# Kernel tuning notes

Measured on AMD Instinct MI355X. Metric: run time of the kernel, lower is better.

## Reference

```python
import jax, jax.numpy as jnp
import numpy as np
from jax import lax


def setup_inputs() -> dict:
    key = jax.random.key(0)
    ks = jax.random.split(key, 8)
    B, N, q = 16, 4096, 256
    sc = float(1.0 / np.sqrt(q))
    return {
        "u": jax.random.normal(ks[0], (B, N, q), jnp.float32),
        "a": jax.random.normal(ks[1], (q,), jnp.float32),  # diag of A
        "W_B": jax.random.normal(ks[2], (q, q), jnp.float32) * sc,
        "b_B": jax.random.normal(ks[3], (q,), jnp.float32) * sc,
        "W_C": jax.random.normal(ks[4], (q, q), jnp.float32) * sc,
        "b_C": jax.random.normal(ks[5], (q,), jnp.float32) * sc,
        "W_D": jax.random.normal(ks[6], (q, q), jnp.float32) * sc,
        "b_D": jax.random.normal(ks[7], (q,), jnp.float32) * sc,
    }


def _solve_im(u, a, W_B, b_B, dt):
    """IM solver. A is diagonal, so M_inv is four diagonal blocks:
    new_x = s*x - dt*s*a*z ; new_z = dt*s*x + s*z, with s = 1/(1+dt^2*a).
    Forcing F = M_inv @ [dt*B(u); 0] -> (dt*s*Bu, dt^2*s*Bu)."""
    s = 1.0 / (1.0 + dt * dt * a)  # (q,)
    Bu = jnp.einsum("bnq,pq->bnp", u, W_B) + b_B  # (B,N,q), torch Linear: u @ W^T + b
    f_x = (dt * s) * Bu
    f_z = (dt * dt * s) * Bu
    dsa = dt * s * a
    ds = dt * s

    def step(carry, f):
        x, z = carry
        fx, fz = f
        x_new = s * x - dsa * z + fx
        z_new = ds * x + s * z + fz
        return (x_new, z_new), z_new

    Bsz, _, q = u.shape
    init = (jnp.zeros((Bsz, q), u.dtype), jnp.zeros((Bsz, q), u.dtype))
    # scan over time axis
    _, z_t = lax.scan(step, init, (jnp.moveaxis(f_x, 1, 0), jnp.moveaxis(f_z, 1, 0)))
    return jnp.moveaxis(z_t, 0, 1)  # (B,N,q) -- the out[..., size:] half


def reference(u, a, W_B, b_B, W_C, b_C, W_D, b_D):
    N = u.shape[1]
    dt = 1.0 / N
    y = _solve_im(u, a, W_B, b_B, dt)
    x = (jnp.einsum("bnq,pq->bnp", y, W_C) + b_C) + (jnp.einsum("bnq,pq->bnp", u, W_D) + b_D)
    x = jax.nn.gelu(x, approximate=False)  # torch GELU default = exact erf
    # GLU(concat([x, x], -1)) == x * sigmoid(x)
    out = x * jax.nn.sigmoid(x) + u
    return (out, y)
```

## Files before the change

kernel.cpp:

```cpp
#include <hip/hip_runtime.h>
#include <hip/hip_bf16.h>
#include <cstdint>

typedef __bf16 bf16_t;
typedef __bf16 bf16x8 __attribute__((ext_vector_type(8)));
typedef float f32x4 __attribute__((ext_vector_type(4)));

#define B_SZ 16
#define N_SZ 4096
#define Q_SZ 256
#define M_TOT (B_SZ * N_SZ)
#define DT (1.0f / 4096.0f)
#define LDST 40
#define CHUNKS 16
#define CLEN (N_SZ / CHUNKS)
#define PF 8


__device__ __forceinline__ bf16x8 load8f(const float* p) {
  const float4 v0 = *(const float4*)p;
  const float4 v1 = *(const float4*)(p + 4);
  bf16x8 v;
  v[0] = (bf16_t)v0.x; v[1] = (bf16_t)v0.y; v[2] = (bf16_t)v0.z; v[3] = (bf16_t)v0.w;
  v[4] = (bf16_t)v1.x; v[5] = (bf16_t)v1.y; v[6] = (bf16_t)v1.z; v[7] = (bf16_t)v1.w;
  return v;
}

__device__ __forceinline__ void gll16(const bf16_t* g, bf16_t* l) {
  __builtin_amdgcn_global_load_lds(
      (const __attribute__((address_space(1))) void*)g,
      (__attribute__((address_space(3))) void*)l, 16, 0, 0);
}


__device__ __forceinline__ void stage2(const bf16_t* __restrict__ A,
                                       const bf16_t* __restrict__ Bm,
                                       int m0, int n0, int k0, int t,
                                       bf16_t* As, bf16_t* Bs) {
#pragma unroll
  for (int j = 0; j < 2; ++j) {
    const int i = j * 256 + t;
    const int row = i >> 2;
    const int cpos = i & 3;
    const int cdat = cpos ^ ((row >> 1) & 3);
    bf16_t* la = As + (size_t)i * 8;
    bf16_t* lb = Bs + (size_t)i * 8;
    gll16(A + (size_t)(m0 + row) * Q_SZ + k0 + cdat * 8, la);
    gll16(Bm + (size_t)(n0 + row) * Q_SZ + k0 + cdat * 8, lb);
  }
}

__device__ __forceinline__ void mstep(const bf16_t* As, const bf16_t* Bs,
                                      int t, f32x4 acc[4][4]) {
  const int lane = t & 63, ln = lane & 15, quad = lane >> 4;
  const int wave = t >> 6;
  const int wm = (wave & 1) * 64, wn = (wave >> 1) * 64;
  const int csw = (quad ^ ((ln >> 1) & 3)) * 8;
  bf16x8 af[4], bv[4];
#pragma unroll
  for (int mi = 0; mi < 4; ++mi) {
    af[mi] = *(const bf16x8*)(As + (wm + mi * 16 + ln) * 32 + csw);
    bv[mi] = *(const bf16x8*)(Bs + (wn + mi * 16 + ln) * 32 + csw);
  }
#pragma unroll
  for (int mi = 0; mi < 4; ++mi)
#pragma unroll
    for (int ni = 0; ni < 4; ++ni)
      acc[mi][ni] = __builtin_amdgcn_mfma_f32_16x16x32_bf16(af[mi], bv[ni],
                                                            acc[mi][ni], 0, 0, 0);
}

__global__ __launch_bounds__(256) void prep_kernel(
    const float* __restrict__ u, const float* __restrict__ WB,
    const float* __restrict__ WC, const float* __restrict__ WD,
    bf16_t* __restrict__ ub, bf16_t* __restrict__ WBb,
    bf16_t* __restrict__ WCb, bf16_t* __restrict__ WDb) {
  const int g = blockIdx.x * 256 + threadIdx.x;
  const int UC = (M_TOT * Q_SZ) / 8;
  const float* src;
  bf16_t* dst;
  int idx;
  if (g < UC) {
    src = u; dst = ub; idx = g;
  } else {
    const int h = g - UC;
    const int w = h >> 13;
    idx = h & 8191;
    src = (w == 0) ? WB : (w == 1) ? WC : WD;
    dst = (w == 0) ? WBb : (w == 1) ? WCb : WDb;
  }
  *(bf16x8*)(dst + (size_t)idx * 8) = load8f(src + (size_t)idx * 8);
}

__global__ __launch_bounds__(256) void gemm1b_kernel(
    const bf16_t* __restrict__ ub, const bf16_t* __restrict__ WBb,
    const float* __restrict__ a, const float* __restrict__ bB,
    float* __restrict__ fx) {
  __shared__ __align__(16) bf16_t As[2][128 * 32];
  __shared__ __align__(16) bf16_t Bs[2][128 * 32];
  const int t = threadIdx.x;
  const int bid = blockIdx.x;
  const int swz = (bid & 7) * 128 + (bid >> 3);
  const int m0 = (swz >> 1) * 128, n0 = (swz & 1) * 128;
  f32x4 acc[4][4] = {};
  stage2(ub, WBb, m0, n0, 0, t, As[0], Bs[0]);
  __syncthreads();
#pragma unroll 2
  for (int k = 0; k < 8; ++k) {
    const int cur = k & 1;
    if (k < 7)
      stage2(ub, WBb, m0, n0, (k + 1) * 32, t, As[cur ^ 1], Bs[cur ^ 1]);
    mstep(As[cur], Bs[cur], t, acc);
    __syncthreads();
  }
  const int lane = t & 63, ln = lane & 15, quad = lane >> 4;
  const int wave = t >> 6;
  const int wm = (wave & 1) * 64, wn = (wave >> 1) * 64;
#pragma unroll
  for (int ni = 0; ni < 4; ++ni) {
    const int gp = n0 + wn + ni * 16 + ln;
    const float av = a[gp];
    const float s = 1.0f / (1.0f + DT * DT * av);
    const float sc = DT * s;
    const float bb = bB[gp];
#pragma unroll
    for (int mi = 0; mi < 4; ++mi) {
      const int gm = m0 + wm + mi * 16 + quad * 4;
#pragma unroll
      for (int r2 = 0; r2 < 4; ++r2)
        fx[(size_t)(gm + r2) * Q_SZ + gp] = sc * (acc[mi][ni][r2] + bb);
    }
  }
}

__global__ __launch_bounds__(256) void gemm2b_kernel(
    const bf16_t* __restrict__ yb, const bf16_t* __restrict__ WCb,
    const bf16_t* __restrict__ ub, const bf16_t* __restrict__ WDb,
    const float* __restrict__ u, const float* __restrict__ bC,
    const float* __restrict__ bD, float* __restrict__ out0) {
  __shared__ __align__(16) bf16_t As[2][128 * 32];
  __shared__ __align__(16) bf16_t Bs[2][128 * 32];
  const int t = threadIdx.x;
  const int bid = blockIdx.x;
  const int swz = (bid & 7) * 128 + (bid >> 3);
  const int m0 = (swz >> 1) * 128, n0 = (swz & 1) * 128;
  f32x4 acc[4][4] = {};
  stage2(yb, WCb, m0, n0, 0, t, As[0], Bs[0]);
  __syncthreads();
#pragma unroll 2
  for (int kk = 0; kk < 16; ++kk) {
    const int cur = kk & 1;
    if (kk < 15) {
      const int nk = kk + 1;
      const bf16_t* Ap = (nk < 8) ? yb : ub;
      const bf16_t* Bp = (nk < 8) ? WCb : WDb;
      stage2(Ap, Bp, m0, n0, (nk & 7) * 32, t, As[cur ^ 1], Bs[cur ^ 1]);
    }
    mstep(As[cur], Bs[cur], t, acc);
    __syncthreads();
  }
  const int lane = t & 63, ln = lane & 15, quad = lane >> 4;
  const int wave = t >> 6;
  const int wm = (wave & 1) * 64, wn = (wave >> 1) * 64;
#pragma unroll
  for (int ni = 0; ni < 4; ++ni) {
    const int gp = n0 + wn + ni * 16 + ln;
    const float bias = bC[gp] + bD[gp];
#pragma unroll
    for (int mi = 0; mi < 4; ++mi) {
      const int gm = m0 + wm + mi * 16 + quad * 4;
#pragma unroll
      for (int r2 = 0; r2 < 4; ++r2) {
        const float x = acc[mi][ni][r2] + bias;
        const float g = 0.5f * x * (1.0f + erff(x * 0.70710678118654752f));
        const float sg = 1.0f / (1.0f + __expf(-g));
        const float uu = u[(size_t)(gm + r2) * Q_SZ + gp];
        out0[(size_t)(gm + r2) * Q_SZ + gp] = fmaf(g, sg, uu);
      }
    }
  }
}


__global__ __launch_bounds__(256) void scan1_kernel(
    const float* __restrict__ fx, const float* __restrict__ a,
    float* __restrict__ ex, float* __restrict__ ez) {
  const int g = blockIdx.x * 256 + threadIdx.x;
  const int p = g & 255, c = (g >> 8) & (CHUNKS - 1), b = g >> 12;
  const float av = a[p];
  const float s = 1.0f / (1.0f + DT * DT * av);
  const float dsa = DT * s * av, dss = DT * s;
  float x = 0.f, z = 0.f;
  const float* fp = fx + ((size_t)b * N_SZ + c * CLEN) * Q_SZ + p;
  float buf[PF], nbuf[PF];
#pragma unroll
  for (int j = 0; j < PF; ++j) buf[j] = fp[(size_t)j * Q_SZ];
  for (int n = 0; n < CLEN; n += PF) {
    if (n + PF < CLEN) {
#pragma unroll
      for (int j = 0; j < PF; ++j) nbuf[j] = fp[(size_t)(n + PF + j) * Q_SZ];
    }
#pragma unroll
    for (int j = 0; j < PF; ++j) {
      const float f = buf[j];
      const float xn = fmaf(s, x, fmaf(-dsa, z, f));
      const float zn = fmaf(dss, x, fmaf(s, z, DT * f));
      x = xn; z = zn;
    }
#pragma unroll
    for (int j = 0; j < PF; ++j) buf[j] = nbuf[j];
  }
  ex[g] = x; ez[g] = z;
}

__global__ __launch_bounds__(256) void scan2_kernel(
    const float* __restrict__ a, const float* __restrict__ ex,
    const float* __restrict__ ez, float* __restrict__ ix, float* __restrict__ iz) {
  const int g = blockIdx.x * 256 + threadIdx.x;
  const int p = g & 255, b = g >> 8;
  const float av = a[p];
  const float s = 1.0f / (1.0f + DT * DT * av);
  float m00 = s, m01 = -DT * s * av, m10 = DT * s, m11 = s;
#pragma unroll
  for (int i = 0; i < 8; ++i) {
    const float a00 = fmaf(m00, m00, m01 * m10);
    const float a01 = m01 * (m00 + m11);
    const float a10 = m10 * (m00 + m11);
    const float a11 = fmaf(m11, m11, m01 * m10);
    m00 = a00; m01 = a01; m10 = a10; m11 = a11;
  }
  float x = 0.f, z = 0.f;
  for (int c = 0; c < CHUNKS; ++c) {
    const size_t idx = ((size_t)b * CHUNKS + c) * Q_SZ + p;
    ix[idx] = x; iz[idx] = z;
    const float xn = fmaf(m00, x, fmaf(m01, z, ex[idx]));
    const float zn = fmaf(m10, x, fmaf(m11, z, ez[idx]));
    x = xn; z = zn;
  }
}

__global__ __launch_bounds__(256) void scan3_kernel(
    const float* __restrict__ a, const float* __restrict__ ix,
    const float* __restrict__ iz, float* __restrict__ yf,
    bf16_t* __restrict__ yb) {
  const int g = blockIdx.x * 256 + threadIdx.x;
  const int p = g & 255, c = (g >> 8) & (CHUNKS - 1), b = g >> 12;
  const float av = a[p];
  const float s = 1.0f / (1.0f + DT * DT * av);
  const float dsa = DT * s * av, dss = DT * s;
  float x = ix[g], z = iz[g];
  const size_t base = ((size_t)b * N_SZ + c * CLEN) * Q_SZ + p;
  float* yp = yf + base;
  bf16_t* ybp = yb ? yb + base : nullptr;
  float buf[PF], nbuf[PF];
#pragma unroll
  for (int j = 0; j < PF; ++j) buf[j] = yp[(size_t)j * Q_SZ];
  for (int n = 0; n < CLEN; n += PF) {
    if (n + PF < CLEN) {
#pragma unroll
      for (int j = 0; j < PF; ++j) nbuf[j] = yp[(size_t)(n + PF + j) * Q_SZ];
    }
#pragma unroll
    for (int j = 0; j < PF; ++j) {
      const float f = buf[j];
      const float xn = fmaf(s, x, fmaf(-dsa, z, f));
      const float zn = fmaf(dss, x, fmaf(s, z, DT * f));
      x = xn; z = zn;
      yp[(size_t)(n + j) * Q_SZ] = zn;
      if (yb) ybp[(size_t)(n + j) * Q_SZ] = (bf16_t)zn;
    }
#pragma unroll
    for (int j = 0; j < PF; ++j) buf[j] = nbuf[j];
  }
}

__global__ __launch_bounds__(256) void scan_mono_kernel(
    const float* __restrict__ a, float* __restrict__ yf) {
  const int g = blockIdx.x * 256 + threadIdx.x;
  const int p = g & 255, b = g >> 8;
  const float av = a[p];
  const float s = 1.0f / (1.0f + DT * DT * av);
  const float dsa = DT * s * av, dss = DT * s;
  float x = 0.f, z = 0.f;
  float* yp = yf + (size_t)b * N_SZ * Q_SZ + p;
  float buf[PF], nbuf[PF];
#pragma unroll
  for (int j = 0; j < PF; ++j) buf[j] = yp[(size_t)j * Q_SZ];
  for (int n = 0; n < N_SZ; n += PF) {
    if (n + PF < N_SZ) {
#pragma unroll
      for (int j = 0; j < PF; ++j) nbuf[j] = yp[(size_t)(n + PF + j) * Q_SZ];
    }
#pragma unroll
    for (int j = 0; j < PF; ++j) {
      const float f = buf[j];
      const float xn = fmaf(s, x, fmaf(-dsa, z, f));
      const float zn = fmaf(dss, x, fmaf(s, z, DT * f));
      x = xn; z = zn;
      yp[(size_t)(n + j) * Q_SZ] = zn;
    }
#pragma unroll
    for (int j = 0; j < PF; ++j) buf[j] = nbuf[j];
  }
}


__device__ __forceinline__ void kloop(const float* __restrict__ Ap,
                                      const float* __restrict__ Bp,
                                      int m0, int n0, int t,
                                      bf16_t* As, bf16_t* Bs, f32x4 acc[4][4]) {
  const int r = t >> 2, cc = t & 3;
  const int lane = t & 63, ln = lane & 15, quad = lane >> 4;
  const int wave = t >> 6;
  const int wm = (wave & 1) * 64, wn = (wave >> 1) * 64;

  for (int k0 = 0; k0 < Q_SZ; k0 += 32) {
#pragma unroll
    for (int i = 0; i < 2; ++i) {
      const int row = r + i * 64;
      const int col = k0 + cc * 8;
      *(bf16x8*)(As + row * LDST + cc * 8) =
          load8f(Ap + (size_t)(m0 + row) * Q_SZ + col);
      *(bf16x8*)(Bs + row * LDST + cc * 8) =
          load8f(Bp + (size_t)(n0 + row) * Q_SZ + col);
    }
    __syncthreads();
    bf16x8 af[4], bv[4];
#pragma unroll
    for (int mi = 0; mi < 4; ++mi) {
      af[mi] = *(const bf16x8*)(As + (wm + mi * 16 + ln) * LDST + quad * 8);
      bv[mi] = *(const bf16x8*)(Bs + (wn + mi * 16 + ln) * LDST + quad * 8);
    }
#pragma unroll
    for (int mi = 0; mi < 4; ++mi)
#pragma unroll
      for (int ni = 0; ni < 4; ++ni)
        acc[mi][ni] = __builtin_amdgcn_mfma_f32_16x16x32_bf16(af[mi], bv[ni],
                                                              acc[mi][ni], 0, 0, 0);
    __syncthreads();
  }
}

__global__ __launch_bounds__(256) void gemm1_kernel(
    const float* __restrict__ u, const float* __restrict__ WB,
    const float* __restrict__ a, const float* __restrict__ bB,
    float* __restrict__ fx) {
  __shared__ __align__(16) bf16_t As[128 * LDST];
  __shared__ __align__(16) bf16_t Bs[128 * LDST];
  const int t = threadIdx.x;
  const int m0 = blockIdx.x * 128, n0 = blockIdx.y * 128;
  f32x4 acc[4][4] = {};
  kloop(u, WB, m0, n0, t, As, Bs, acc);

  const int lane = t & 63, ln = lane & 15, quad = lane >> 4;
  const int wave = t >> 6;
  const int wm = (wave & 1) * 64, wn = (wave >> 1) * 64;
#pragma unroll
  for (int ni = 0; ni < 4; ++ni) {
    const int gp = n0 + wn + ni * 16 + ln;
    const float av = a[gp];
    const float s = 1.0f / (1.0f + DT * DT * av);
    const float sc = DT * s;
    const float bb = bB[gp];
#pragma unroll
    for (int mi = 0; mi < 4; ++mi) {
      const int gm = m0 + wm + mi * 16 + quad * 4;
#pragma unroll
      for (int r2 = 0; r2 < 4; ++r2)
        fx[(size_t)(gm + r2) * Q_SZ + gp] = sc * (acc[mi][ni][r2] + bb);
    }
  }
}

__global__ __launch_bounds__(256) void gemm2_kernel(
    const float* __restrict__ y, const float* __restrict__ WC,
    const float* __restrict__ u, const float* __restrict__ WD,
    const float* __restrict__ bC, const float* __restrict__ bD,
    float* __restrict__ out0) {
  __shared__ __align__(16) bf16_t As[128 * LDST];
  __shared__ __align__(16) bf16_t Bs[128 * LDST];
  const int t = threadIdx.x;
  const int m0 = blockIdx.x * 128, n0 = blockIdx.y * 128;
  f32x4 acc[4][4] = {};
  kloop(y, WC, m0, n0, t, As, Bs, acc);
  kloop(u, WD, m0, n0, t, As, Bs, acc);

  const int lane = t & 63, ln = lane & 15, quad = lane >> 4;
  const int wave = t >> 6;
  const int wm = (wave & 1) * 64, wn = (wave >> 1) * 64;
#pragma unroll
  for (int ni = 0; ni < 4; ++ni) {
    const int gp = n0 + wn + ni * 16 + ln;
    const float bias = bC[gp] + bD[gp];
#pragma unroll
    for (int mi = 0; mi < 4; ++mi) {
      const int gm = m0 + wm + mi * 16 + quad * 4;
#pragma unroll
      for (int r2 = 0; r2 < 4; ++r2) {
        const float x = acc[mi][ni][r2] + bias;
        const float g = 0.5f * x * (1.0f + erff(x * 0.70710678118654752f));
        const float sg = 1.0f / (1.0f + __expf(-g));
        const float uu = u[(size_t)(gm + r2) * Q_SZ + gp];
        out0[(size_t)(gm + r2) * Q_SZ + gp] = fmaf(g, sg, uu);
      }
    }
  }
}


extern "C" void kernel_launch(void* const* d_in, const int* in_sizes, int n_in,
                              void* d_out, int out_size, void* d_ws, size_t ws_size,
                              hipStream_t stream) {
  const float* u  = (const float*)d_in[0];
  const float* a  = (const float*)d_in[1];
  const float* WB = (const float*)d_in[2];
  const float* bB = (const float*)d_in[3];
  const float* WC = (const float*)d_in[4];
  const float* bC = (const float*)d_in[5];
  const float* WD = (const float*)d_in[6];
  const float* bD = (const float*)d_in[7];

  float* out0 = (float*)d_out;
  float* yreg = out0 + (size_t)M_TOT * Q_SZ;

  const size_t UB_ELEMS = (size_t)M_TOT * Q_SZ;
  const size_t W_ELEMS = (size_t)Q_SZ * Q_SZ;
  const size_t state_bytes = 4 * (size_t)M_TOT * sizeof(float);
  const size_t need_full =
      (2 * UB_ELEMS + 3 * W_ELEMS) * sizeof(bf16_t) + state_bytes;

  if (ws_size >= need_full) {
    bf16_t* ub  = (bf16_t*)d_ws;
    bf16_t* yb  = ub + UB_ELEMS;
    bf16_t* WBb = yb + UB_ELEMS;
    bf16_t* WCb = WBb + W_ELEMS;
    bf16_t* WDb = WCb + W_ELEMS;
    float* ex = (float*)(WDb + W_ELEMS);
    float* ez = ex + M_TOT;
    float* ix = ez + M_TOT;
    float* iz = ix + M_TOT;

    prep_kernel<<<8288, 256, 0, stream>>>(u, WB, WC, WD, ub, WBb, WCb, WDb);
    gemm1b_kernel<<<1024, 256, 0, stream>>>(ub, WBb, a, bB, yreg);
    scan1_kernel<<<256, 256, 0, stream>>>(yreg, a, ex, ez);
    scan2_kernel<<<16, 256, 0, stream>>>(a, ex, ez, ix, iz);
    scan3_kernel<<<256, 256, 0, stream>>>(a, ix, iz, yreg, yb);
    gemm2b_kernel<<<1024, 256, 0, stream>>>(yb, WCb, ub, WDb, u, bC, bD, out0);
  } else {
    dim3 gg(M_TOT / 128, Q_SZ / 128);
    gemm1_kernel<<<gg, 256, 0, stream>>>(u, WB, a, bB, yreg);
    if (ws_size >= state_bytes) {
      float* ex = (float*)d_ws;
      float* ez = ex + M_TOT;
      float* ix = ez + M_TOT;
      float* iz = ix + M_TOT;
      scan1_kernel<<<256, 256, 0, stream>>>(yreg, a, ex, ez);
      scan2_kernel<<<16, 256, 0, stream>>>(a, ex, ez, ix, iz);
      scan3_kernel<<<256, 256, 0, stream>>>(a, ix, iz, yreg, (bf16_t*)nullptr);
    } else {
      scan_mono_kernel<<<16, 256, 0, stream>>>(a, yreg);
    }
    gemm2_kernel<<<gg, 256, 0, stream>>>(yreg, WC, u, WD, bC, bD, out0);
  }
}
```

Baseline: 357.4 us.

## Drop u bf16 prep, use LDS-free direct-load GEMMs, and quadruple scan chunks

Removes the full bf16 conversion pass over u. The GEMM kernels now load fp32 u directly from global memory into registers, converting on the fly, instead of staging bf16 tiles through LDS with async loads. Scan chunk count rises from 16 to 64, quadrupling scan1/scan3 parallelism and shrinking sequential length per thread; state buffers are resized to match. The trade-off is losing LDS reuse: each wave reloads its A and B fragments from global/L2, and fp32 u is read twice rather than once in bf16.

Result: slower. 414.8 us (+16.1%).

```diff
diff --git a/kernel.cpp b/kernel.cpp
--- a/kernel.cpp
+++ b/kernel.cpp
@@ -12,7 +12,8 @@
 #define M_TOT (B_SZ * N_SZ)
 #define DT (1.0f / 4096.0f)
 #define LDST 40
-#define CHUNKS 16
+#define CHUNKS 64
+#define LOG2_CLEN 6
 #define CLEN (N_SZ / CHUNKS)
 #define PF 8
 
@@ -26,96 +27,59 @@
   return v;
 }
 
-__device__ __forceinline__ void gll16(const bf16_t* g, bf16_t* l) {
-  __builtin_amdgcn_global_load_lds(
-      (const __attribute__((address_space(1))) void*)g,
-      (__attribute__((address_space(3))) void*)l, 16, 0, 0);
-}
-
-
-__device__ __forceinline__ void stage2(const bf16_t* __restrict__ A,
-                                       const bf16_t* __restrict__ Bm,
-                                       int m0, int n0, int k0, int t,
-                                       bf16_t* As, bf16_t* Bs) {
-#pragma unroll
-  for (int j = 0; j < 2; ++j) {
-    const int i = j * 256 + t;
-    const int row = i >> 2;
-    const int cpos = i & 3;
-    const int cdat = cpos ^ ((row >> 1) & 3);
-    bf16_t* la = As + (size_t)i * 8;
-    bf16_t* lb = Bs + (size_t)i * 8;
-    gll16(A + (size_t)(m0 + row) * Q_SZ + k0 + cdat * 8, la);
-    gll16(Bm + (size_t)(n0 + row) * Q_SZ + k0 + cdat * 8, lb);
-  }
-}
-
-__device__ __forceinline__ void mstep(const bf16_t* As, const bf16_t* Bs,
-                                      int t, f32x4 acc[4][4]) {
-  const int lane = t & 63, ln = lane & 15, quad = lane >> 4;
-  const int wave = t >> 6;
-  const int wm = (wave & 1) * 64, wn = (wave >> 1) * 64;
-  const int csw = (quad ^ ((ln >> 1) & 3)) * 8;
-  bf16x8 af[4], bv[4];
-#pragma unroll
-  for (int mi = 0; mi < 4; ++mi) {
-    af[mi] = *(const bf16x8*)(As + (wm + mi * 16 + ln) * 32 + csw);
-    bv[mi] = *(const bf16x8*)(Bs + (wn + mi * 16 + ln) * 32 + csw);
-  }
-#pragma unroll
-  for (int mi = 0; mi < 4; ++mi)
-#pragma unroll
-    for (int ni = 0; ni < 4; ++ni)
-      acc[mi][ni] = __builtin_amdgcn_mfma_f32_16x16x32_bf16(af[mi], bv[ni],
-                                                            acc[mi][ni], 0, 0, 0);
-}
-
-__global__ __launch_bounds__(256) void prep_kernel(
-    const float* __restrict__ u, const float* __restrict__ WB,
-    const float* __restrict__ WC, const float* __restrict__ WD,
-    bf16_t* __restrict__ ub, bf16_t* __restrict__ WBb,
+template <bool A_F32>
+__device__ __forceinline__ void kpass(const void* __restrict__ Aptr,
+                                      const bf16_t* __restrict__ Bw,
+                                      int aRow0, int bRow0, int ln, int quad,
+                                      f32x4 acc[4][4]) {
+#pragma unroll
+  for (int k0 = 0; k0 < Q_SZ; k0 += 32) {
+    bf16x8 af[4], bv[4];
+#pragma unroll
+    for (int i = 0; i < 4; ++i) {
+      if constexpr (A_F32) {
+        af[i] = load8f((const float*)Aptr +
+                       (size_t)(aRow0 + i * 16 + ln) * Q_SZ + k0 + quad * 8);
+      } else {
+        af[i] = *(const bf16x8*)((const bf16_t*)Aptr +
+                                 (size_t)(aRow0 + i * 16 + ln) * Q_SZ + k0 + quad * 8);
+      }
+      bv[i] = *(const bf16x8*)(Bw + (size_t)(bRow0 + i * 16 + ln) * Q_SZ + k0 + quad * 8);
+    }
+#pragma unroll
+    for (int mi = 0; mi < 4; ++mi)
+#pragma unroll
+      for (int ni = 0; ni < 4; ++ni)
+        acc[mi][ni] = __builtin_amdgcn_mfma_f32_16x16x32_bf16(af[mi], bv[ni],
+                                                              acc[mi][ni], 0, 0, 0);
+  }
+}
+
+__global__ __launch_bounds__(256) void prepw_kernel(
+    const float* __restrict__ WB, const float* __restrict__ WC,
+    const float* __restrict__ WD, bf16_t* __restrict__ WBb,
     bf16_t* __restrict__ WCb, bf16_t* __restrict__ WDb) {
   const int g = blockIdx.x * 256 + threadIdx.x;
-  const int UC = (M_TOT * Q_SZ) / 8;
-  const float* src;
-  bf16_t* dst;
-  int idx;
-  if (g < UC) {
-    src = u; dst = ub; idx = g;
-  } else {
-    const int h = g - UC;
-    const int w = h >> 13;
-    idx = h & 8191;
-    src = (w == 0) ? WB : (w == 1) ? WC : WD;
-    dst = (w == 0) ? WBb : (w == 1) ? WCb : WDb;
-  }
+  const int w = g >> 13;
+  const int idx = g & 8191;
+  const float* src = (w == 0) ? WB : (w == 1) ? WC : WD;
+  bf16_t* dst = (w == 0) ? WBb : (w == 1) ? WCb : WDb;
   *(bf16x8*)(dst + (size_t)idx * 8) = load8f(src + (size_t)idx * 8);
 }
 
-__global__ __launch_bounds__(256) void gemm1b_kernel(
-    const bf16_t* __restrict__ ub, const bf16_t* __restrict__ WBb,
+__global__ __launch_bounds__(256, 3) void gemm1d_kernel(
+    const float* __restrict__ u, const bf16_t* __restrict__ WBb,
     const float* __restrict__ a, const float* __restrict__ bB,
     float* __restrict__ fx) {
-  __shared__ __align__(16) bf16_t As[2][128 * 32];
-  __shared__ __align__(16) bf16_t Bs[2][128 * 32];
   const int t = threadIdx.x;
   const int bid = blockIdx.x;
   const int swz = (bid & 7) * 128 + (bid >> 3);
   const int m0 = (swz >> 1) * 128, n0 = (swz & 1) * 128;
-  f32x4 acc[4][4] = {};
-  stage2(ub, WBb, m0, n0, 0, t, As[0], Bs[0]);
-  __syncthreads();
-#pragma unroll 2
-  for (int k = 0; k < 8; ++k) {
-    const int cur = k & 1;
-    if (k < 7)
-      stage2(ub, WBb, m0, n0, (k + 1) * 32, t, As[cur ^ 1], Bs[cur ^ 1]);
-    mstep(As[cur], Bs[cur], t, acc);
-    __syncthreads();
-  }
   const int lane = t & 63, ln = lane & 15, quad = lane >> 4;
   const int wave = t >> 6;
   const int wm = (wave & 1) * 64, wn = (wave >> 1) * 64;
+  f32x4 acc[4][4] = {};
+  kpass<true>(u, WBb, m0 + wm, n0 + wn, ln, quad, acc);
 #pragma unroll
   for (int ni = 0; ni < 4; ++ni) {
     const int gp = n0 + wn + ni * 16 + ln;
@@ -133,35 +97,21 @@
   }
 }
 
-__global__ __launch_bounds__(256) void gemm2b_kernel(
+__global__ __launch_bounds__(256, 3) void gemm2d_kernel(
     const bf16_t* __restrict__ yb, const bf16_t* __restrict__ WCb,
-    const bf16_t* __restrict__ ub, const bf16_t* __restrict__ WDb,
-    const float* __restrict__ u, const float* __restrict__ bC,
-    const float* __restrict__ bD, float* __restrict__ out0) {
-  __shared__ __align__(16) bf16_t As[2][128 * 32];
-  __shared__ __align__(16) bf16_t Bs[2][128 * 32];
+    const float* __restrict__ u, const bf16_t* __restrict__ WDb,
+    const float* __restrict__ bC, const float* __restrict__ bD,
+    float* __restrict__ out0) {
   const int t = threadIdx.x;
   const int bid = blockIdx.x;
   const int swz = (bid & 7) * 128 + (bid >> 3);
   const int m0 = (swz >> 1) * 128, n0 = (swz & 1) * 128;
-  f32x4 acc[4][4] = {};
-  stage2(yb, WCb, m0, n0, 0, t, As[0], Bs[0]);
-  __syncthreads();
-#pragma unroll 2
-  for (int kk = 0; kk < 16; ++kk) {
-    const int cur = kk & 1;
-    if (kk < 15) {
-      const int nk = kk + 1;
-      const bf16_t* Ap = (nk < 8) ? yb : ub;
-      const bf16_t* Bp = (nk < 8) ? WCb : WDb;
-      stage2(Ap, Bp, m0, n0, (nk & 7) * 32, t, As[cur ^ 1], Bs[cur ^ 1]);
-    }
-    mstep(As[cur], Bs[cur], t, acc);
-    __syncthreads();
-  }
   const int lane = t & 63, ln = lane & 15, quad = lane >> 4;
   const int wave = t >> 6;
   const int wm = (wave & 1) * 64, wn = (wave >> 1) * 64;
+  f32x4 acc[4][4] = {};
+  kpass<false>(yb, WCb, m0 + wm, n0 + wn, ln, quad, acc);
+  kpass<true>(u, WDb, m0 + wm, n0 + wn, ln, quad, acc);
 #pragma unroll
   for (int ni = 0; ni < 4; ++ni) {
     const int gp = n0 + wn + ni * 16 + ln;
@@ -186,7 +136,7 @@
     const float* __restrict__ fx, const float* __restrict__ a,
     float* __restrict__ ex, float* __restrict__ ez) {
   const int g = blockIdx.x * 256 + threadIdx.x;
-  const int p = g & 255, c = (g >> 8) & (CHUNKS - 1), b = g >> 12;
+  const int p = g & 255, c = (g >> 8) & (CHUNKS - 1), b = g >> 14;
   const float av = a[p];
   const float s = 1.0f / (1.0f + DT * DT * av);
   const float dsa = DT * s * av, dss = DT * s;
@@ -222,7 +172,7 @@
   const float s = 1.0f / (1.0f + DT * DT * av);
   float m00 = s, m01 = -DT * s * av, m10 = DT * s, m11 = s;
 #pragma unroll
-  for (int i = 0; i < 8; ++i) {
+  for (int i = 0; i < LOG2_CLEN; ++i) {
     const float a00 = fmaf(m00, m00, m01 * m10);
     const float a01 = m01 * (m00 + m11);
     const float a10 = m10 * (m00 + m11);
@@ -244,7 +194,7 @@
     const float* __restrict__ iz, float* __restrict__ yf,
     bf16_t* __restrict__ yb) {
   const int g = blockIdx.x * 256 + threadIdx.x;
-  const int p = g & 255, c = (g >> 8) & (CHUNKS - 1), b = g >> 12;
+  const int p = g & 255, c = (g >> 8) & (CHUNKS - 1), b = g >> 14;
   const float av = a[p];
   const float s = 1.0f / (1.0f + DT * DT * av);
   const float dsa = DT * s * av, dss = DT * s;
@@ -425,38 +375,38 @@
 
   const size_t UB_ELEMS = (size_t)M_TOT * Q_SZ;
   const size_t W_ELEMS = (size_t)Q_SZ * Q_SZ;
-  const size_t state_bytes = 4 * (size_t)M_TOT * sizeof(float);
+  const size_t state_bytes =
+      4 * (size_t)B_SZ * CHUNKS * Q_SZ * sizeof(float);
   const size_t need_full =
-      (2 * UB_ELEMS + 3 * W_ELEMS) * sizeof(bf16_t) + state_bytes;
+      (UB_ELEMS + 3 * W_ELEMS) * sizeof(bf16_t) + state_bytes;
 
   if (ws_size >= need_full) {
-    bf16_t* ub  = (bf16_t*)d_ws;
-    bf16_t* yb  = ub + UB_ELEMS;
+    bf16_t* yb  = (bf16_t*)d_ws;
     bf16_t* WBb = yb + UB_ELEMS;
     bf16_t* WCb = WBb + W_ELEMS;
     bf16_t* WDb = WCb + W_ELEMS;
     float* ex = (float*)(WDb + W_ELEMS);
-    float* ez = ex + M_TOT;
-    float* ix = ez + M_TOT;
-    float* iz = ix + M_TOT;
-
-    prep_kernel<<<8288, 256, 0, stream>>>(u, WB, WC, WD, ub, WBb, WCb, WDb);
-    gemm1b_kernel<<<1024, 256, 0, stream>>>(ub, WBb, a, bB, yreg);
-    scan1_kernel<<<256, 256, 0, stream>>>(yreg, a, ex, ez);
+    float* ez = ex + (size_t)B_SZ * CHUNKS * Q_SZ;
+    float* ix = ez + (size_t)B_SZ * CHUNKS * Q_SZ;
+    float* iz = ix + (size_t)B_SZ * CHUNKS * Q_SZ;
+
+    prepw_kernel<<<96, 256, 0, stream>>>(WB, WC, WD, WBb, WCb, WDb);
+    gemm1d_kernel<<<1024, 256, 0, stream>>>(u, WBb, a, bB, yreg);
+    scan1_kernel<<<1024, 256, 0, stream>>>(yreg, a, ex, ez);
     scan2_kernel<<<16, 256, 0, stream>>>(a, ex, ez, ix, iz);
-    scan3_kernel<<<256, 256, 0, stream>>>(a, ix, iz, yreg, yb);
-    gemm2b_kernel<<<1024, 256, 0, stream>>>(yb, WCb, ub, WDb, u, bC, bD, out0);
+    scan3_kernel<<<1024, 256, 0, stream>>>(a, ix, iz, yreg, yb);
+    gemm2d_kernel<<<1024, 256, 0, stream>>>(yb, WCb, u, WDb, bC, bD, out0);
   } else {
     dim3 gg(M_TOT / 128, Q_SZ / 128);
     gemm1_kernel<<<gg, 256, 0, stream>>>(u, WB, a, bB, yreg);
     if (ws_size >= state_bytes) {
       float* ex = (float*)d_ws;
-      float* ez = ex + M_TOT;
-      float* ix = ez + M_TOT;
-      float* iz = ix + M_TOT;
-      scan1_kernel<<<256, 256, 0, stream>>>(yreg, a, ex, ez);
+      float* ez = ex + (size_t)B_SZ * CHUNKS * Q_SZ;
+      float* ix = ez + (size_t)B_SZ * CHUNKS * Q_SZ;
+      float* iz = ix + (size_t)B_SZ * CHUNKS * Q_SZ;
+      scan1_kernel<<<1024, 256, 0, stream>>>(yreg, a, ex, ez);
       scan2_kernel<<<16, 256, 0, stream>>>(a, ex, ez, ix, iz);
-      scan3_kernel<<<256, 256, 0, stream>>>(a, ix, iz, yreg, (bf16_t*)nullptr);
+      scan3_kernel<<<1024, 256, 0, stream>>>(a, ix, iz, yreg, (bf16_t*)nullptr);
     } else {
       scan_mono_kernel<<<16, 256, 0, stream>>>(a, yreg);
     }
```
